# Optimization experiments

Hardware: AMD Instinct MI355X
Metric: run time of the kernel (lower is better)

## Reference

```python
import jax, jax.numpy as jnp
import numpy as np

M, K, N = 4096, 4096, 11008  # tokens, in_features, out_features


def setup_inputs() -> dict:
    key = jax.random.key(0)
    k0, k1, k2 = jax.random.split(key, 3)
    # quint8 activations: values in [0, 255], zero_point 128
    x_q = jax.random.randint(k0, (M, K), 0, 256, dtype=jnp.int32)
    # qint8 weight: values in [-128, 127], zero_point 0 (as prepacked in __init__)
    w_q = jax.random.randint(k1, (N, K), -128, 128, dtype=jnp.int32)
    bias = jax.random.normal(k2, (N,), dtype=jnp.float32) * 0.1
    return {
        "x_q": x_q,
        "w_q": w_q,
        "bias": bias,
        "x_scale": jnp.float32(0.02),
        "w_scale": jnp.float32(0.01),
        "out_scale": jnp.float32(1.0),   # self.scale = 1.0
        "x_zero_point": 128,
        "out_zero_point": 0,             # self.zero_point = 0
    }


def reference(x_q, w_q, bias, x_scale, w_scale, out_scale, x_zero_point, out_zero_point):
    # int8 GEMM with int32 accumulation: (x - zp_x) @ W^T
    acc = jnp.einsum(
        "mk,nk->mn",
        x_q - x_zero_point,
        w_q,
        preferred_element_type=jnp.int32,
    )
    # dequantize + bias (fp32), then requantize to quint8 output
    y = acc.astype(jnp.float32) * (x_scale * w_scale) + bias
    q = jnp.clip(jnp.round(y / out_scale) + out_zero_point, 0, 255).astype(jnp.int32)
    return q
```

## Files before the change

kernel.cpp:

```cpp
#include <hip/hip_runtime.h>

#define M_DIM 4096
#define K_DIM 4096
#define N_DIM 11008
#define BM 128
#define BN 128
#define BK 128
#define NTILES (K_DIM / BK)

typedef int v4i  __attribute__((ext_vector_type(4)));
typedef int v16i __attribute__((ext_vector_type(16)));

#define WAIT_VM8 0x3F78
#define WAIT_VM0 0x3F70

__device__ __forceinline__ void load_lds16(const void* g, void* l) {
    __builtin_amdgcn_global_load_lds(
        (const __attribute__((address_space(1))) void*)g,
        (__attribute__((address_space(3))) void*)l,
        16, 0, 0);
}

__global__ void pack_x_kernel(const int* __restrict__ x, signed char* __restrict__ out,
                              const int* __restrict__ zp_p, int n4) {
    int i = blockIdx.x * blockDim.x + threadIdx.x;
    if (i >= n4) return;
    int zp = zp_p[0];
    int4 v = ((const int4*)x)[i];
    unsigned int p = ((unsigned int)(v.x - zp) & 0xFF)
                   | (((unsigned int)(v.y - zp) & 0xFF) << 8)
                   | (((unsigned int)(v.z - zp) & 0xFF) << 16)
                   | (((unsigned int)(v.w - zp) & 0xFF) << 24);
    ((unsigned int*)out)[i] = p;
}

__global__ void pack_w_kernel(const int* __restrict__ w, signed char* __restrict__ out, int n4) {
    int i = blockIdx.x * blockDim.x + threadIdx.x;
    if (i >= n4) return;
    int4 v = ((const int4*)w)[i];
    unsigned int p = ((unsigned int)v.x & 0xFF)
                   | (((unsigned int)v.y & 0xFF) << 8)
                   | (((unsigned int)v.z & 0xFF) << 16)
                   | (((unsigned int)v.w & 0xFF) << 24);
    ((unsigned int*)out)[i] = p;
}

__global__ __launch_bounds__(256) void gemm_i8_kernel(
    const signed char* __restrict__ A8,
    const signed char* __restrict__ B8,
    const float* __restrict__ bias,
    const float* __restrict__ xs_p, const float* __restrict__ ws_p,
    const float* __restrict__ os_p, const int* __restrict__ ozp_p,
    int* __restrict__ out) {
    __shared__ v4i As0[BM * BK / 16];
    __shared__ v4i Bs0[BN * BK / 16];
    __shared__ v4i As1[BM * BK / 16];
    __shared__ v4i Bs1[BN * BK / 16];

    const int tid  = threadIdx.x;
    const int lane = tid & 63;
    const int wave = tid >> 6;

    const int bid   = blockIdx.x;
    const int xcd   = bid & 7;
    const int local = bid >> 3;
    const int m_blk = xcd * 4 + (local & 3);
    const int n_blk = (local >> 4) * 4 + ((local & 15) >> 2);
    const int m0 = m_blk * BM;
    const int n0 = n_blk * BN;

    long offA[4], offB[4];
    int  ldsOff[4];
#pragma unroll
    for (int j = 0; j < 4; ++j) {
        const int s   = tid + 256 * j;
        const int row = s >> 3;
        const int gg  = (s & 7) ^ (row & 7);
        offA[j]   = (long)(m0 + row) * K_DIM + gg * 16;
        offB[j]   = (long)(n0 + row) * K_DIM + gg * 16;
        ldsOff[j] = s;
    }

    const int waveM = wave >> 1, waveN = wave & 1;
    const int l31 = lane & 31, h = lane >> 5;
    int aSlot[2][4], bSlot[2][4];
#pragma unroll
    for (int t = 0; t < 2; ++t) {
        const int rA = waveM * 64 + t * 32 + l31;
        const int rB = waveN * 64 + t * 32 + l31;
#pragma unroll
        for (int s = 0; s < 4; ++s) {
            const int g = 2 * s + h;
            aSlot[t][s] = rA * 8 + (g ^ (rA & 7));
            bSlot[t][s] = rB * 8 + (g ^ (rB & 7));
        }
    }

    v16i acc[2][2];
#pragma unroll
    for (int mt = 0; mt < 2; ++mt)
#pragma unroll
        for (int nt = 0; nt < 2; ++nt)
#pragma unroll
            for (int r = 0; r < 16; ++r) acc[mt][nt][r] = 0;

    auto stage = [&](int tile, v4i* Asb, v4i* Bsb) {
        const long koff = (long)tile * BK;
#pragma unroll
        for (int j = 0; j < 4; ++j) load_lds16(A8 + offA[j] + koff, (char*)(Asb + ldsOff[j]));
#pragma unroll
        for (int j = 0; j < 4; ++j) load_lds16(B8 + offB[j] + koff, (char*)(Bsb + ldsOff[j]));
    };
    auto compute = [&](const v4i* Asb, const v4i* Bsb) {
#pragma unroll
        for (int s = 0; s < 4; ++s) {
            v4i a[2], b[2];
#pragma unroll
            for (int t = 0; t < 2; ++t) a[t] = Asb[aSlot[t][s]];
#pragma unroll
            for (int t = 0; t < 2; ++t) b[t] = Bsb[bSlot[t][s]];
#pragma unroll
            for (int mt = 0; mt < 2; ++mt)
#pragma unroll
                for (int nt = 0; nt < 2; ++nt)
                    acc[mt][nt] = __builtin_amdgcn_mfma_i32_32x32x32_i8(
                        a[mt], b[nt], acc[mt][nt], 0, 0, 0);
        }
    };

    stage(0, As0, Bs0);
    stage(1, As1, Bs1);

#pragma unroll 1
    for (int kk = 0; kk < 15; ++kk) {
        const int k = 2 * kk;
        __builtin_amdgcn_s_waitcnt(WAIT_VM8);
        __builtin_amdgcn_s_barrier();
        compute(As0, Bs0);
        __builtin_amdgcn_s_barrier();
        stage(k + 2, As0, Bs0);
        __builtin_amdgcn_s_waitcnt(WAIT_VM8);
        __builtin_amdgcn_s_barrier();
        compute(As1, Bs1);
        __builtin_amdgcn_s_barrier();
        stage(k + 3, As1, Bs1);
    }
    __builtin_amdgcn_s_waitcnt(WAIT_VM8);
    __builtin_amdgcn_s_barrier();
    compute(As0, Bs0);
    __builtin_amdgcn_s_waitcnt(WAIT_VM0);
    __builtin_amdgcn_s_barrier();
    compute(As1, Bs1);

    const float scale  = xs_p[0] * ws_p[0];
    const float inv_os = 1.0f / os_p[0];
    const int   ozp    = ozp_p[0];
#pragma unroll
    for (int mt = 0; mt < 2; ++mt) {
        const int rbase = m0 + waveM * 64 + mt * 32 + 4 * h;
#pragma unroll
        for (int nt = 0; nt < 2; ++nt) {
            const int col = n0 + waveN * 64 + nt * 32 + l31;
            const float bv = bias[col];
#pragma unroll
            for (int r = 0; r < 16; ++r) {
                const int row = rbase + (r & 3) + 8 * (r >> 2);
                float y = (float)acc[mt][nt][r] * scale + bv;
                int q = (int)rintf(y * inv_os) + ozp;
                q = q < 0 ? 0 : (q > 255 ? 255 : q);
                out[(long)row * N_DIM + col] = q;
            }
        }
    }
}

extern "C" void kernel_launch(void* const* d_in, const int* in_sizes, int n_in,
                              void* d_out, int out_size, void* d_ws, size_t ws_size,
                              hipStream_t stream) {
    const int*   x_q  = (const int*)d_in[0];
    const int*   w_q  = (const int*)d_in[1];
    const float* bias = (const float*)d_in[2];
    const float* xs   = (const float*)d_in[3];
    const float* wsc  = (const float*)d_in[4];
    const float* os   = (const float*)d_in[5];
    const int*   xzp  = (const int*)d_in[6];
    const int*   ozp  = (const int*)d_in[7];

    signed char* x8 = (signed char*)d_ws;
    signed char* w8 = (signed char*)d_ws + (size_t)M_DIM * K_DIM;

    const int nx4 = M_DIM * K_DIM / 4;
    pack_x_kernel<<<(nx4 + 255) / 256, 256, 0, stream>>>(x_q, x8, xzp, nx4);
    const int nw4 = N_DIM * K_DIM / 4;
    pack_w_kernel<<<(nw4 + 255) / 256, 256, 0, stream>>>(w_q, w8, nw4);

    const int nblocks = (M_DIM / BM) * (N_DIM / BN);
    gemm_i8_kernel<<<nblocks, 256, 0, stream>>>(x8, w8, bias, xs, wsc, os, ozp, (int*)d_out);
}
```

Before: 517.2 us.

## Enlarge GEMM tiles to 256x256 with 8 waves and vectorize pack kernels

Raises the block tile from 128x128 to 256x256 and uses 512 threads (8 waves, 2x4), each wave now computing a 128x64 sub-tile. The block-to-tile mapping is rebuilt so each XCD owns two M rows of 43 N tiles. The aim is more reuse of each staged tile and fewer global loads per MFMA. The compute loop adds per-step barriers and s_setprio around the MFMA bursts to keep waves in lockstep, replacing the separate post-compute barriers. The int8 pack kernels now handle 16 elements per thread with 16-byte stores. The trade-off is a 128KB LDS footprint and higher register pressure, which limit occupancy to one block per CU.

```diff
diff --git a/kernel.cpp b/kernel.cpp
--- a/kernel.cpp
+++ b/kernel.cpp
@@ -3,8 +3,8 @@
 #define M_DIM 4096
 #define K_DIM 4096
 #define N_DIM 11008
-#define BM 128
-#define BN 128
+#define BM 256
+#define BN 256
 #define BK 128
 #define NTILES (K_DIM / BK)
 
@@ -21,31 +21,40 @@
         16, 0, 0);
 }
 
-__global__ void pack_x_kernel(const int* __restrict__ x, signed char* __restrict__ out,
-                              const int* __restrict__ zp_p, int n4) {
+__device__ __forceinline__ unsigned int pack4(int4 v, int zp) {
+    return ((unsigned int)(v.x - zp) & 0xFF)
+         | (((unsigned int)(v.y - zp) & 0xFF) << 8)
+         | (((unsigned int)(v.z - zp) & 0xFF) << 16)
+         | (((unsigned int)(v.w - zp) & 0xFF) << 24);
+}
+
+__global__ void pack_x_kernel(const int* __restrict__ x, unsigned int* __restrict__ out,
+                              const int* __restrict__ zp_p, int n16) {
     int i = blockIdx.x * blockDim.x + threadIdx.x;
-    if (i >= n4) return;
-    int zp = zp_p[0];
-    int4 v = ((const int4*)x)[i];
-    unsigned int p = ((unsigned int)(v.x - zp) & 0xFF)
-                   | (((unsigned int)(v.y - zp) & 0xFF) << 8)
-                   | (((unsigned int)(v.z - zp) & 0xFF) << 16)
-                   | (((unsigned int)(v.w - zp) & 0xFF) << 24);
-    ((unsigned int*)out)[i] = p;
-}
-
-__global__ void pack_w_kernel(const int* __restrict__ w, signed char* __restrict__ out, int n4) {
+    if (i >= n16) return;
+    const int zp = zp_p[0];
+    const int4* p = (const int4*)x + i * 4;
+    uint4 o;
+    o.x = pack4(p[0], zp);
+    o.y = pack4(p[1], zp);
+    o.z = pack4(p[2], zp);
+    o.w = pack4(p[3], zp);
+    ((uint4*)out)[i] = o;
+}
+
+__global__ void pack_w_kernel(const int* __restrict__ w, unsigned int* __restrict__ out, int n16) {
     int i = blockIdx.x * blockDim.x + threadIdx.x;
-    if (i >= n4) return;
-    int4 v = ((const int4*)w)[i];
-    unsigned int p = ((unsigned int)v.x & 0xFF)
-                   | (((unsigned int)v.y & 0xFF) << 8)
-                   | (((unsigned int)v.z & 0xFF) << 16)
-                   | (((unsigned int)v.w & 0xFF) << 24);
-    ((unsigned int*)out)[i] = p;
-}
-
-__global__ __launch_bounds__(256) void gemm_i8_kernel(
+    if (i >= n16) return;
+    const int4* p = (const int4*)w + i * 4;
+    uint4 o;
+    o.x = pack4(p[0], 0);
+    o.y = pack4(p[1], 0);
+    o.z = pack4(p[2], 0);
+    o.w = pack4(p[3], 0);
+    ((uint4*)out)[i] = o;
+}
+
+__global__ __launch_bounds__(512, 2) void gemm_i8_kernel(
     const signed char* __restrict__ A8,
     const signed char* __restrict__ B8,
     const float* __restrict__ bias,
@@ -64,8 +73,8 @@
     const int bid   = blockIdx.x;
     const int xcd   = bid & 7;
     const int local = bid >> 3;
-    const int m_blk = xcd * 4 + (local & 3);
-    const int n_blk = (local >> 4) * 4 + ((local & 15) >> 2);
+    const int m_blk = xcd * 2 + (local >= 43 ? 1 : 0);
+    const int n_blk = (local >= 43) ? (local - 43) : local;
     const int m0 = m_blk * BM;
     const int n0 = n_blk * BN;
 
@@ -73,7 +82,7 @@
     int  ldsOff[4];
 #pragma unroll
     for (int j = 0; j < 4; ++j) {
-        const int s   = tid + 256 * j;
+        const int s   = tid + 512 * j;
         const int row = s >> 3;
         const int gg  = (s & 7) ^ (row & 7);
         offA[j]   = (long)(m0 + row) * K_DIM + gg * 16;
@@ -81,24 +90,31 @@
         ldsOff[j] = s;
     }
 
-    const int waveM = wave >> 1, waveN = wave & 1;
+    const int waveM = wave >> 2, waveN = wave & 3;
     const int l31 = lane & 31, h = lane >> 5;
-    int aSlot[2][4], bSlot[2][4];
-#pragma unroll
-    for (int t = 0; t < 2; ++t) {
-        const int rA = waveM * 64 + t * 32 + l31;
-        const int rB = waveN * 64 + t * 32 + l31;
+    int aSlot[4][4], bSlot[2][4];
+#pragma unroll
+    for (int mt = 0; mt < 4; ++mt) {
+        const int rA = waveM * 128 + mt * 32 + l31;
 #pragma unroll
         for (int s = 0; s < 4; ++s) {
             const int g = 2 * s + h;
-            aSlot[t][s] = rA * 8 + (g ^ (rA & 7));
-            bSlot[t][s] = rB * 8 + (g ^ (rB & 7));
-        }
-    }
-
-    v16i acc[2][2];
-#pragma unroll
-    for (int mt = 0; mt < 2; ++mt)
+            aSlot[mt][s] = rA * 8 + (g ^ (rA & 7));
+        }
+    }
+#pragma unroll
+    for (int nt = 0; nt < 2; ++nt) {
+        const int rB = waveN * 64 + nt * 32 + l31;
+#pragma unroll
+        for (int s = 0; s < 4; ++s) {
+            const int g = 2 * s + h;
+            bSlot[nt][s] = rB * 8 + (g ^ (rB & 7));
+        }
+    }
+
+    v16i acc[4][2];
+#pragma unroll
+    for (int mt = 0; mt < 4; ++mt)
 #pragma unroll
         for (int nt = 0; nt < 2; ++nt)
 #pragma unroll
@@ -111,20 +127,25 @@
 #pragma unroll
         for (int j = 0; j < 4; ++j) load_lds16(B8 + offB[j] + koff, (char*)(Bsb + ldsOff[j]));
     };
+
     auto compute = [&](const v4i* Asb, const v4i* Bsb) {
 #pragma unroll
         for (int s = 0; s < 4; ++s) {
-            v4i a[2], b[2];
-#pragma unroll
-            for (int t = 0; t < 2; ++t) a[t] = Asb[aSlot[t][s]];
-#pragma unroll
-            for (int t = 0; t < 2; ++t) b[t] = Bsb[bSlot[t][s]];
-#pragma unroll
-            for (int mt = 0; mt < 2; ++mt)
+            v4i a[4], b[2];
+#pragma unroll
+            for (int mt = 0; mt < 4; ++mt) a[mt] = Asb[aSlot[mt][s]];
+#pragma unroll
+            for (int nt = 0; nt < 2; ++nt) b[nt] = Bsb[bSlot[nt][s]];
+            __builtin_amdgcn_s_barrier();
+            __builtin_amdgcn_s_setprio(1);
+#pragma unroll
+            for (int mt = 0; mt < 4; ++mt)
 #pragma unroll
                 for (int nt = 0; nt < 2; ++nt)
                     acc[mt][nt] = __builtin_amdgcn_mfma_i32_32x32x32_i8(
                         a[mt], b[nt], acc[mt][nt], 0, 0, 0);
+            __builtin_amdgcn_s_setprio(0);
+            __builtin_amdgcn_s_barrier();
         }
     };
 
@@ -137,12 +158,10 @@
         __builtin_amdgcn_s_waitcnt(WAIT_VM8);
         __builtin_amdgcn_s_barrier();
         compute(As0, Bs0);
-        __builtin_amdgcn_s_barrier();
         stage(k + 2, As0, Bs0);
         __builtin_amdgcn_s_waitcnt(WAIT_VM8);
         __builtin_amdgcn_s_barrier();
         compute(As1, Bs1);
-        __builtin_amdgcn_s_barrier();
         stage(k + 3, As1, Bs1);
     }
     __builtin_amdgcn_s_waitcnt(WAIT_VM8);
@@ -156,8 +175,8 @@
     const float inv_os = 1.0f / os_p[0];
     const int   ozp    = ozp_p[0];
 #pragma unroll
-    for (int mt = 0; mt < 2; ++mt) {
-        const int rbase = m0 + waveM * 64 + mt * 32 + 4 * h;
+    for (int mt = 0; mt < 4; ++mt) {
+        const int rbase = m0 + waveM * 128 + mt * 32 + 4 * h;
 #pragma unroll
         for (int nt = 0; nt < 2; ++nt) {
             const int col = n0 + waveN * 64 + nt * 32 + l31;
@@ -189,11 +208,11 @@
     signed char* x8 = (signed char*)d_ws;
     signed char* w8 = (signed char*)d_ws + (size_t)M_DIM * K_DIM;
 
-    const int nx4 = M_DIM * K_DIM / 4;
-    pack_x_kernel<<<(nx4 + 255) / 256, 256, 0, stream>>>(x_q, x8, xzp, nx4);
-    const int nw4 = N_DIM * K_DIM / 4;
-    pack_w_kernel<<<(nw4 + 255) / 256, 256, 0, stream>>>(w_q, w8, nw4);
+    const int nx16 = M_DIM * K_DIM / 16;
+    pack_x_kernel<<<(nx16 + 255) / 256, 256, 0, stream>>>(x_q, (unsigned int*)x8, xzp, nx16);
+    const int nw16 = N_DIM * K_DIM / 16;
+    pack_w_kernel<<<(nw16 + 255) / 256, 256, 0, stream>>>(w_q, (unsigned int*)w8, nw16);
 
     const int nblocks = (M_DIM / BM) * (N_DIM / BN);
-    gemm_i8_kernel<<<nblocks, 256, 0, stream>>>(x8, w8, bias, xs, wsc, os, ozp, (int*)d_out);
-}
+    gemm_i8_kernel<<<nblocks, 512, 0, stream>>>(x8, w8, bias, xs, wsc, os, ozp, (int*)d_out);
+}
```

Measured after the change: 555.7 us. +7.4%, slower.
